# Performance work log

Measured on AMD Instinct MI355X. Metric: run time of the kernel, lower is better.

## Reference

```python
import jax, jax.numpy as jnp
import numpy as np
from jax import lax

B, C, H, W = 32, 3, 256, 256
P, D, E, K = 16, 256, 8, 2
HP, WP = H // P, W // P
N = HP * WP
GATE_IN = C * P * P  # 768
GATE_HID = D // 2    # 128


def _mk(key, shape, scale=0.02):
    return scale * jax.random.normal(key, shape, dtype=jnp.float32)


def setup_inputs() -> dict:
    key = jax.random.key(0)
    ks = jax.random.split(key, 20)
    inp = {
        "x": jax.random.normal(ks[0], (B, C, H, W), dtype=jnp.float32),
        # gate MLP: Linear(768,128) -> ReLU -> Linear(128,8)
        "g_w1": _mk(ks[1], (GATE_HID, GATE_IN)),
        "g_b1": jnp.zeros((GATE_HID,), jnp.float32),
        "g_w2": _mk(ks[2], (E, GATE_HID)),
        "g_b2": jnp.zeros((E,), jnp.float32),
        # per-expert CNN params, stacked with leading expert dim E
        "dw1_w": _mk(ks[3], (E, 3, 1, 3, 3)),   "dw1_b": jnp.zeros((E, 3), jnp.float32),
        "pw1_w": _mk(ks[4], (E, 64, 3, 1, 1)),  "pw1_b": jnp.zeros((E, 64), jnp.float32),
        "dw2_w": _mk(ks[5], (E, 64, 1, 3, 3)),  "dw2_b": jnp.zeros((E, 64), jnp.float32),
        "pw2_w": _mk(ks[6], (E, 128, 64, 1, 1)), "pw2_b": jnp.zeros((E, 128), jnp.float32),
        "dw3_w": _mk(ks[7], (E, 128, 1, 3, 3)), "dw3_b": jnp.zeros((E, 128), jnp.float32),
        "pw3_w": _mk(ks[8], (E, D, 128, 1, 1)), "pw3_b": jnp.zeros((E, D), jnp.float32),
    }
    return inp


def _dwconv(x, w, b, stride):
    # depthwise 3x3, padding 1; x: [n, c, h, w]; w: [c, 1, 3, 3]
    c = x.shape[1]
    y = lax.conv_general_dilated(
        x, w, (stride, stride), ((1, 1), (1, 1)),
        dimension_numbers=("NCHW", "OIHW", "NCHW"), feature_group_count=c)
    return jax.nn.relu(y + b[None, :, None, None])


def _pwconv(x, w, b):
    # pointwise 1x1 conv as GEMM; w: [o, c, 1, 1]
    y = jnp.einsum("nchw,oc->nohw", x, w[:, :, 0, 0]) + b[None, :, None, None]
    return jax.nn.relu(y)


def _expert(x, dw1w, dw1b, pw1w, pw1b, dw2w, dw2b, pw2w, pw2b, dw3w, dw3b, pw3w, pw3b):
    # x: [BN, 3, 16, 16] -> [BN, D]
    x = _pwconv(_dwconv(x, dw1w, dw1b, 2), pw1w, pw1b)   # [BN, 64, 8, 8]
    x = _pwconv(_dwconv(x, dw2w, dw2b, 2), pw2w, pw2b)   # [BN, 128, 4, 4]
    x = _pwconv(_dwconv(x, dw3w, dw3b, 2), pw3w, pw3b)   # [BN, 256, 2, 2]
    return x.mean(axis=(2, 3))                            # adaptive avg pool to 1x1


def reference(x, g_w1, g_b1, g_w2, g_b2,
              dw1_w, dw1_b, pw1_w, pw1_b, dw2_w, dw2_b, pw2_w, pw2_b,
              dw3_w, dw3_b, pw3_w, pw3_b):
    b = x.shape[0]
    # nn.Unfold(kernel=P, stride=P): columns ordered (c, di, dj)
    patches = x.reshape(b, C, HP, P, WP, P).transpose(0, 2, 4, 1, 3, 5)  # [B,hp,wp,C,P,P]
    patches_sp = patches.reshape(b * N, C, P, P)
    patches_flat = patches_sp.reshape(b * N, GATE_IN)

    # gate (eval mode: dropout is identity)
    h = jax.nn.relu(patches_flat @ g_w1.T + g_b1)
    logits = h @ g_w2.T + g_b2                       # [BN, E]
    topk_vals, topk_idx = lax.top_k(logits, K)       # [BN, K]
    weights = jax.nn.softmax(topk_vals, axis=-1)
    one_hot = jax.nn.one_hot(topk_idx, E, dtype=x.dtype)   # [BN, K, E]
    routing = (one_hot * weights[..., None]).sum(axis=1)   # [BN, E]

    # run all experts densely (as the original does), then combine
    expert_outs = jax.vmap(_expert, in_axes=(None,) + (0,) * 12)(
        patches_sp, dw1_w, dw1_b, pw1_w, pw1_b, dw2_w, dw2_b,
        pw2_w, pw2_b, dw3_w, dw3_b, pw3_w, pw3_b)   # [E, BN, D]
    out = jnp.einsum("ne,end->nd", routing, expert_outs)  # [BN, D]

    features = out.reshape(b, HP, WP, D).transpose(0, 3, 1, 2)  # [B, D, hp, wp]
    load_balance_loss = jnp.float32(0.0)  # eval mode
    return features, load_balance_loss
```

## Files before the change

### kernel.cpp

```cpp
#include <hip/hip_runtime.h>

#define BN 8192
#define GIN 768

#define O_ROUTE_I 0UL
#define O_ROUTE_W (O_ROUTE_I + (size_t)BN*2*4)
#define O_COUNTS  (O_ROUTE_W + (size_t)BN*2*4)
#define O_LISTS   (O_COUNTS + 256)
#define O_PW2T    (O_LISTS + (size_t)8*BN*4)
#define O_PW3T    (O_PW2T + (size_t)8*64*128*4)
#define O_SLOT    (O_PW3T + (size_t)8*128*256*4)

__global__ __launch_bounds__(256) void k0_prep(const float* __restrict__ pw2w,
                                               const float* __restrict__ pw3w,
                                               float* __restrict__ pw2t,
                                               float* __restrict__ pw3t,
                                               int* __restrict__ counts)
{
    int tid = blockIdx.x * 256 + threadIdx.x;
    if (tid < 8) counts[tid] = 0;
    for (int idx = tid; idx < 8 * 128 * 64; idx += 256 * 256) {
        int e = idx >> 13; int r = idx & 8191; int oc = r >> 6; int c = r & 63;
        pw2t[(size_t)e * 8192 + c * 128 + oc] = pw2w[idx];
    }
    for (int idx = tid; idx < 8 * 256 * 128; idx += 256 * 256) {
        int e = idx >> 15; int r = idx & 32767; int oc = r >> 7; int c = r & 127;
        pw3t[(size_t)e * 32768 + c * 256 + oc] = pw3w[idx];
    }
}

__global__ __launch_bounds__(256) void k1_gate(
    const float* __restrict__ x, const float* __restrict__ w1,
    const float* __restrict__ b1, const float* __restrict__ w2,
    const float* __restrict__ b2,
    int* __restrict__ route_i, float* __restrict__ route_w,
    int* __restrict__ counts, int* __restrict__ lists)
{
    __shared__ __align__(16) float A[32][44];
    __shared__ __align__(16) float Wl[32][132];
    __shared__ float hl[32][132];
    __shared__ float ll[32][8];

    int tid = threadIdx.x;
    int pblk = blockIdx.x * 32;

    int pgrp = tid & 7;
    int hgrp = tid >> 3;
    float acc[4][4] = {};

    int sp  = tid >> 3;
    int sk4 = (tid & 7) * 4;
    int swh = tid >> 1;
    int swk = (tid & 1) * 16;

    int patchA = pblk + sp;
    int bA = patchA >> 8; int nA = patchA & 255; int hpA = nA >> 4; int wpA = nA & 15;

    for (int kc = 0; kc < GIN; kc += 32) {
        {
            int k = kc + sk4;
            int c = k >> 8; int rem = k & 255; int ri = rem >> 4; int j = rem & 15;
            const float* src = x + (((size_t)(bA * 3 + c) * 256 + hpA * 16 + ri) * 256 + wpA * 16 + j);
            float4 a4 = *reinterpret_cast<const float4*>(src);
            A[sk4 + 0][sp] = a4.x; A[sk4 + 1][sp] = a4.y;
            A[sk4 + 2][sp] = a4.z; A[sk4 + 3][sp] = a4.w;
        }
        {
            const float* wsrc = w1 + (size_t)swh * GIN + kc + swk;
            #pragma unroll
            for (int q = 0; q < 4; q++) {
                float4 w4 = *reinterpret_cast<const float4*>(wsrc + q * 4);
                Wl[swk + q * 4 + 0][swh] = w4.x; Wl[swk + q * 4 + 1][swh] = w4.y;
                Wl[swk + q * 4 + 2][swh] = w4.z; Wl[swk + q * 4 + 3][swh] = w4.w;
            }
        }
        __syncthreads();
        float cacc[4][4] = {};
        #pragma unroll
        for (int k2 = 0; k2 < 32; k2++) {
            float4 av = *reinterpret_cast<const float4*>(&A[k2][pgrp * 4]);
            float4 wv = *reinterpret_cast<const float4*>(&Wl[k2][hgrp * 4]);
            float aa[4] = {av.x, av.y, av.z, av.w};
            float ww[4] = {wv.x, wv.y, wv.z, wv.w};
            #pragma unroll
            for (int i = 0; i < 4; i++) {
                #pragma unroll
                for (int jj = 0; jj < 4; jj++) cacc[i][jj] += aa[i] * ww[jj];
            }
        }
        #pragma unroll
        for (int i = 0; i < 4; i++) {
            #pragma unroll
            for (int jj = 0; jj < 4; jj++) acc[i][jj] += cacc[i][jj];
        }
        __syncthreads();
    }

    #pragma unroll
    for (int jj = 0; jj < 4; jj++) {
        float bb = b1[hgrp * 4 + jj];
        #pragma unroll
        for (int i = 0; i < 4; i++) {
            float v = acc[i][jj] + bb;
            hl[pgrp * 4 + i][hgrp * 4 + jj] = v > 0.f ? v : 0.f;
        }
    }
    __syncthreads();

    {
        int lp = tid >> 3; int le = tid & 7;
        float lacc = b2[le];
        const float* wrow = w2 + le * 128;
        for (int h = 0; h < 128; h++) lacc += hl[lp][h] * wrow[h];
        ll[lp][le] = lacc;
    }
    __syncthreads();

    if (tid < 32) {
        int patch = pblk + tid;
        float v[8];
        #pragma unroll
        for (int e = 0; e < 8; e++) v[e] = ll[tid][e];
        int e0 = 0; float m0 = v[0];
        #pragma unroll
        for (int e = 1; e < 8; e++) if (v[e] > m0) { m0 = v[e]; e0 = e; }
        int e1 = -1; float m1 = -3.0e38f;
        #pragma unroll
        for (int e = 0; e < 8; e++) if (e != e0 && v[e] > m1) { m1 = v[e]; e1 = e; }
        float t = expf(m1 - m0);
        float w0 = 1.f / (1.f + t);
        float w1v = t * w0;
        route_i[patch * 2] = e0; route_i[patch * 2 + 1] = e1;
        route_w[patch * 2] = w0; route_w[patch * 2 + 1] = w1v;
        int p0 = atomicAdd(&counts[e0], 1);
        lists[e0 * BN + p0] = patch * 2;
        int p1 = atomicAdd(&counts[e1], 1);
        lists[e1 * BN + p1] = patch * 2 + 1;
    }
}

__global__ __launch_bounds__(256, 4) void k23_expert(
    const float* __restrict__ x, const int* __restrict__ counts,
    const int* __restrict__ lists,
    const float* __restrict__ dw1w, const float* __restrict__ dw1b,
    const float* __restrict__ pw1w, const float* __restrict__ pw1b,
    const float* __restrict__ dw2w, const float* __restrict__ dw2b,
    const float* __restrict__ pw2t, const float* __restrict__ pw2b,
    const float* __restrict__ dw3w, const float* __restrict__ dw3b,
    const float* __restrict__ pw3t, const float* __restrict__ pw3b,
    float* __restrict__ slot)
{
    __shared__ __align__(16) float buf[4][2560];

    int e = blockIdx.x & 7;
    int chunk = blockIdx.x >> 3;
    int cnt = counts[e];
    int base = chunk * 4;
    if (base >= cnt) return;
    int tid = threadIdx.x;
    int en = tid >> 6; int l = tid & 63;
    if (base + en >= cnt) return;
    int pslot = lists[e * BN + base + en];
    int patch = pslot >> 1;
    int b = patch >> 8, nn = patch & 255, hp = nn >> 4, wp = nn & 15;

    float* pl  = buf[en];
    float* d1  = buf[en] + 2048;
    float* d2t = buf[en];
    float* p2  = buf[en];
    float* d3  = buf[en] + 2048;

    {
        int r = l >> 2; int j4 = (l & 3) * 4;
        #pragma unroll
        for (int c = 0; c < 3; c++) {
            const float* src = x + (((size_t)(b * 3 + c) * 256 + hp * 16 + r) * 256 + wp * 16 + j4);
            float4 v = *reinterpret_cast<const float4*>(src);
            *reinterpret_cast<float4*>(&pl[c * 320 + r * 20 + j4]) = v;
        }
    }

    {
        int oh = l >> 3, ow = l & 7;
        #pragma unroll
        for (int c = 0; c < 3; c++) {
            const float* w9 = dw1w + (e * 3 + c) * 9;
            float acc = dw1b[e * 3 + c];
            #pragma unroll
            for (int ki = 0; ki < 3; ki++) {
                int ih = oh * 2 - 1 + ki;
                if ((unsigned)ih < 16u) {
                    #pragma unroll
                    for (int kj = 0; kj < 3; kj++) {
                        int iw = ow * 2 - 1 + kj;
                        if ((unsigned)iw < 16u) acc += pl[c * 320 + ih * 20 + iw] * w9[ki * 3 + kj];
                    }
                }
            }
            d1[c * 64 + l] = acc > 0.f ? acc : 0.f;
        }
    }

    {
        const float* w3 = pw1w + (e * 64 + l) * 3;
        float pw0 = w3[0], pw1v = w3[1], pw2v = w3[2];
        float pb = pw1b[e * 64 + l];
        const float* w9 = dw2w + (e * 64 + l) * 9;
        float wd[9];
        #pragma unroll
        for (int i = 0; i < 9; i++) wd[i] = w9[i];
        float bd = dw2b[e * 64 + l];

        float rc[8] = {};
        float re[8], ro[8];

        #pragma unroll
        for (int oh = 0; oh < 4; oh++) {
            #pragma unroll
            for (int half = 0; half < 2; half++) {
                float* dst = half ? ro : re;
                const float* d1b = d1 + (oh * 2 + half) * 8;
                float4 x0 = *reinterpret_cast<const float4*>(&d1b[0]);
                float4 x1 = *reinterpret_cast<const float4*>(&d1b[4]);
                float4 y0 = *reinterpret_cast<const float4*>(&d1b[64]);
                float4 y1 = *reinterpret_cast<const float4*>(&d1b[68]);
                float4 z0 = *reinterpret_cast<const float4*>(&d1b[128]);
                float4 z1 = *reinterpret_cast<const float4*>(&d1b[132]);
                float v;
                v = pb + x0.x * pw0 + y0.x * pw1v + z0.x * pw2v; dst[0] = v > 0.f ? v : 0.f;
                v = pb + x0.y * pw0 + y0.y * pw1v + z0.y * pw2v; dst[1] = v > 0.f ? v : 0.f;
                v = pb + x0.z * pw0 + y0.z * pw1v + z0.z * pw2v; dst[2] = v > 0.f ? v : 0.f;
                v = pb + x0.w * pw0 + y0.w * pw1v + z0.w * pw2v; dst[3] = v > 0.f ? v : 0.f;
                v = pb + x1.x * pw0 + y1.x * pw1v + z1.x * pw2v; dst[4] = v > 0.f ? v : 0.f;
                v = pb + x1.y * pw0 + y1.y * pw1v + z1.y * pw2v; dst[5] = v > 0.f ? v : 0.f;
                v = pb + x1.z * pw0 + y1.z * pw1v + z1.z * pw2v; dst[6] = v > 0.f ? v : 0.f;
                v = pb + x1.w * pw0 + y1.w * pw1v + z1.w * pw2v; dst[7] = v > 0.f ? v : 0.f;
            }
            #pragma unroll
            for (int ow = 0; ow < 4; ow++) {
                float acc = bd;
                if (oh > 0) {
                    #pragma unroll
                    for (int kj = 0; kj < 3; kj++) {
                        int iw = ow * 2 - 1 + kj;
                        if ((unsigned)iw < 8u) acc += rc[iw] * wd[kj];
                    }
                }
                #pragma unroll
                for (int kj = 0; kj < 3; kj++) {
                    int iw = ow * 2 - 1 + kj;
                    if ((unsigned)iw < 8u) acc += re[iw] * wd[3 + kj];
                }
                #pragma unroll
                for (int kj = 0; kj < 3; kj++) {
                    int iw = ow * 2 - 1 + kj;
                    if ((unsigned)iw < 8u) acc += ro[iw] * wd[6 + kj];
                }
                d2t[(oh * 4 + ow) * 68 + l] = acc > 0.f ? acc : 0.f;
            }
            #pragma unroll
            for (int i = 0; i < 8; i++) rc[i] = ro[i];
        }
    }

    {
        int ocg = l & 15; int pq = l >> 4;
        int oc0 = ocg * 8; int p0 = pq * 4;
        float acc[8][4] = {};
        const float* wbase = pw2t + (size_t)e * 8192;
        for (int c4 = 0; c4 < 16; c4++) {
            float4 a0 = *reinterpret_cast<const float4*>(&d2t[(p0 + 0) * 68 + c4 * 4]);
            float4 a1 = *reinterpret_cast<const float4*>(&d2t[(p0 + 1) * 68 + c4 * 4]);
            float4 a2 = *reinterpret_cast<const float4*>(&d2t[(p0 + 2) * 68 + c4 * 4]);
            float4 a3 = *reinterpret_cast<const float4*>(&d2t[(p0 + 3) * 68 + c4 * 4]);
            float av[4][4] = {{a0.x, a1.x, a2.x, a3.x}, {a0.y, a1.y, a2.y, a3.y},
                              {a0.z, a1.z, a2.z, a3.z}, {a0.w, a1.w, a2.w, a3.w}};
            #pragma unroll
            for (int cc = 0; cc < 4; cc++) {
                int c = c4 * 4 + cc;
                float4 wa = *reinterpret_cast<const float4*>(wbase + c * 128 + oc0);
                float4 wb = *reinterpret_cast<const float4*>(wbase + c * 128 + oc0 + 4);
                float wv[8] = {wa.x, wa.y, wa.z, wa.w, wb.x, wb.y, wb.z, wb.w};
                #pragma unroll
                for (int j = 0; j < 8; j++) {
                    #pragma unroll
                    for (int i = 0; i < 4; i++) acc[j][i] += wv[j] * av[cc][i];
                }
            }
        }
        #pragma unroll
        for (int j = 0; j < 8; j++) {
            float bb = pw2b[e * 128 + oc0 + j];
            #pragma unroll
            for (int i = 0; i < 4; i++) {
                float v = acc[j][i] + bb;
                p2[(oc0 + j) * 16 + ((p0 + i + ocg) & 15)] = v > 0.f ? v : 0.f;
            }
        }
    }

    {
        #pragma unroll
        for (int chb = 0; chb < 128; chb += 64) {
            int ch = chb + l;
            int grp = ch >> 3;
            const float* w9 = dw3w + (e * 128 + ch) * 9;
            float bb = dw3b[e * 128 + ch];
            #pragma unroll
            for (int pos = 0; pos < 4; pos++) {
                int oh = pos >> 1, ow = pos & 1;
                float acc = bb;
                #pragma unroll
                for (int ki = 0; ki < 3; ki++) {
                    int ih = oh * 2 - 1 + ki;
                    if ((unsigned)ih < 4u) {
                        #pragma unroll
                        for (int kj = 0; kj < 3; kj++) {
                            int iw = ow * 2 - 1 + kj;
                            if ((unsigned)iw < 4u)
                                acc += p2[ch * 16 + ((ih * 4 + iw + grp) & 15)] * w9[ki * 3 + kj];
                        }
                    }
                }
                d3[ch * 4 + pos] = acc > 0.f ? acc : 0.f;
            }
        }
    }

    {
        int oc0 = l * 4;
        const float* wbase = pw3t + (size_t)e * 32768;
        float acc[4][4] = {};
        for (int c = 0; c < 128; c++) {
            float4 a = *reinterpret_cast<const float4*>(&d3[c * 4]);
            float4 w = *reinterpret_cast<const float4*>(wbase + c * 256 + oc0);
            float av[4] = {a.x, a.y, a.z, a.w};
            float wv[4] = {w.x, w.y, w.z, w.w};
            #pragma unroll
            for (int j = 0; j < 4; j++) {
                #pragma unroll
                for (int i = 0; i < 4; i++) acc[j][i] += wv[j] * av[i];
            }
        }
        float o4[4];
        #pragma unroll
        for (int j = 0; j < 4; j++) {
            float bb = pw3b[e * 256 + oc0 + j];
            float s = 0.f;
            #pragma unroll
            for (int i = 0; i < 4; i++) {
                float v = acc[j][i] + bb;
                s += (v > 0.f ? v : 0.f);
            }
            o4[j] = 0.25f * s;
        }
        *reinterpret_cast<float4*>(slot + (size_t)pslot * 256 + oc0) =
            make_float4(o4[0], o4[1], o4[2], o4[3]);
    }
}

__global__ __launch_bounds__(256) void k4_comb(
    const float* __restrict__ slot, const float* __restrict__ route_w,
    float* __restrict__ out)
{
    __shared__ float cl[16][257];
    int bx = blockIdx.x;
    int b = bx >> 4; int hp = bx & 15;
    int tid = threadIdx.x;
    int d = tid;
    for (int wp = 0; wp < 16; wp++) {
        int n = (b * 16 + hp) * 16 + wp;
        float w0 = route_w[n * 2], w1 = route_w[n * 2 + 1];
        float v = w0 * slot[(size_t)(n * 2) * 256 + d] + w1 * slot[(size_t)(n * 2 + 1) * 256 + d];
        cl[wp][d] = v;
    }
    __syncthreads();
    int wp = tid & 15; int dg = tid >> 4;
    for (int r = 0; r < 16; r++) {
        int dd = r * 16 + dg;
        out[(((size_t)b * 256 + dd) * 16 + hp) * 16 + wp] = cl[wp][dd];
    }
    if (bx == 0 && tid == 0) out[(size_t)BN * 256] = 0.0f;
}

extern "C" void kernel_launch(void* const* d_in, const int* in_sizes, int n_in,
                              void* d_out, int out_size, void* d_ws, size_t ws_size,
                              hipStream_t stream)
{
    const float* x    = (const float*)d_in[0];
    const float* gw1  = (const float*)d_in[1];
    const float* gb1  = (const float*)d_in[2];
    const float* gw2  = (const float*)d_in[3];
    const float* gb2  = (const float*)d_in[4];
    const float* dw1w = (const float*)d_in[5];
    const float* dw1b = (const float*)d_in[6];
    const float* pw1w = (const float*)d_in[7];
    const float* pw1b = (const float*)d_in[8];
    const float* dw2w = (const float*)d_in[9];
    const float* dw2b = (const float*)d_in[10];
    const float* pw2w = (const float*)d_in[11];
    const float* pw2b = (const float*)d_in[12];
    const float* dw3w = (const float*)d_in[13];
    const float* dw3b = (const float*)d_in[14];
    const float* pw3w = (const float*)d_in[15];
    const float* pw3b = (const float*)d_in[16];

    char* ws = (char*)d_ws;
    int*   route_i = (int*)(ws + O_ROUTE_I);
    float* route_w = (float*)(ws + O_ROUTE_W);
    int*   counts  = (int*)(ws + O_COUNTS);
    int*   lists   = (int*)(ws + O_LISTS);
    float* pw2t    = (float*)(ws + O_PW2T);
    float* pw3t    = (float*)(ws + O_PW3T);
    float* slot    = (float*)(ws + O_SLOT);
    float* out     = (float*)d_out;

    hipLaunchKernelGGL(k0_prep, dim3(256), dim3(256), 0, stream,
                       pw2w, pw3w, pw2t, pw3t, counts);
    hipLaunchKernelGGL(k1_gate, dim3(BN / 32), dim3(256), 0, stream,
                       x, gw1, gb1, gw2, gb2, route_i, route_w, counts, lists);
    hipLaunchKernelGGL(k23_expert, dim3(8 * 2048), dim3(256), 0, stream,
                       x, counts, lists, dw1w, dw1b, pw1w, pw1b, dw2w, dw2b,
                       pw2t, pw2b, dw3w, dw3b, pw3t, pw3b, slot);
    hipLaunchKernelGGL(k4_comb, dim3(512), dim3(256), 0, stream,
                       slot, route_w, out);
}
```

Before: 532.0 us.

## Share expert pointwise GEMM weights across patches in block and shrink gate tile

In the expert kernel, the pw2 and pw3 pointwise GEMMs are repartitioned. Each wavefront now computes a slice of output channels for all four patches in the block, reading the other wavefronts' activations through shared memory. Before, each wavefront owned one patch and read the full weight matrix. This cuts per-block global weight traffic about fourfold, at the cost of added __syncthreads and rotated/skewed shared-memory indexing to avoid bank conflicts. The gate kernel tile is also halved to 16 patches per block, doubling the grid for more parallelism.

```diff
diff --git a/kernel.cpp b/kernel.cpp
--- a/kernel.cpp
+++ b/kernel.cpp
@@ -2,6 +2,7 @@
 
 #define BN 8192
 #define GIN 768
+#define SL 2560
 
 #define O_ROUTE_I 0UL
 #define O_ROUTE_W (O_ROUTE_I + (size_t)BN*2*4)
@@ -36,20 +37,20 @@
     int* __restrict__ route_i, float* __restrict__ route_w,
     int* __restrict__ counts, int* __restrict__ lists)
 {
-    __shared__ __align__(16) float A[32][44];
+    __shared__ __align__(16) float A[32][20];
     __shared__ __align__(16) float Wl[32][132];
-    __shared__ float hl[32][132];
-    __shared__ float ll[32][8];
+    __shared__ float hl[16][132];
+    __shared__ float ll[16][8];
 
     int tid = threadIdx.x;
-    int pblk = blockIdx.x * 32;
+    int pblk = blockIdx.x * 16;
 
     int pgrp = tid & 7;
     int hgrp = tid >> 3;
-    float acc[4][4] = {};
-
-    int sp  = tid >> 3;
-    int sk4 = (tid & 7) * 4;
+    float acc[2][4] = {};
+
+    int sp  = tid >> 4;
+    int sk2 = (tid & 15) * 2;
     int swh = tid >> 1;
     int swk = (tid & 1) * 16;
 
@@ -58,38 +59,37 @@
 
     for (int kc = 0; kc < GIN; kc += 32) {
         {
-            int k = kc + sk4;
+            int k = kc + sk2;
             int c = k >> 8; int rem = k & 255; int ri = rem >> 4; int j = rem & 15;
             const float* src = x + (((size_t)(bA * 3 + c) * 256 + hpA * 16 + ri) * 256 + wpA * 16 + j);
-            float4 a4 = *reinterpret_cast<const float4*>(src);
-            A[sk4 + 0][sp] = a4.x; A[sk4 + 1][sp] = a4.y;
-            A[sk4 + 2][sp] = a4.z; A[sk4 + 3][sp] = a4.w;
+            float2 a2 = *reinterpret_cast<const float2*>(src);
+            A[sk2][sp] = a2.x; A[sk2 + 1][sp] = a2.y;
         }
         {
             const float* wsrc = w1 + (size_t)swh * GIN + kc + swk;
             #pragma unroll
-            for (int q = 0; q < 4; q++) {
-                float4 w4 = *reinterpret_cast<const float4*>(wsrc + q * 4);
-                Wl[swk + q * 4 + 0][swh] = w4.x; Wl[swk + q * 4 + 1][swh] = w4.y;
-                Wl[swk + q * 4 + 2][swh] = w4.z; Wl[swk + q * 4 + 3][swh] = w4.w;
+            for (int qq = 0; qq < 4; qq++) {
+                float4 w4 = *reinterpret_cast<const float4*>(wsrc + qq * 4);
+                Wl[swk + qq * 4 + 0][swh] = w4.x; Wl[swk + qq * 4 + 1][swh] = w4.y;
+                Wl[swk + qq * 4 + 2][swh] = w4.z; Wl[swk + qq * 4 + 3][swh] = w4.w;
             }
         }
         __syncthreads();
-        float cacc[4][4] = {};
+        float cacc[2][4] = {};
         #pragma unroll
         for (int k2 = 0; k2 < 32; k2++) {
-            float4 av = *reinterpret_cast<const float4*>(&A[k2][pgrp * 4]);
+            float2 av = *reinterpret_cast<const float2*>(&A[k2][pgrp * 2]);
             float4 wv = *reinterpret_cast<const float4*>(&Wl[k2][hgrp * 4]);
-            float aa[4] = {av.x, av.y, av.z, av.w};
+            float aa[2] = {av.x, av.y};
             float ww[4] = {wv.x, wv.y, wv.z, wv.w};
             #pragma unroll
-            for (int i = 0; i < 4; i++) {
+            for (int i = 0; i < 2; i++) {
                 #pragma unroll
                 for (int jj = 0; jj < 4; jj++) cacc[i][jj] += aa[i] * ww[jj];
             }
         }
         #pragma unroll
-        for (int i = 0; i < 4; i++) {
+        for (int i = 0; i < 2; i++) {
             #pragma unroll
             for (int jj = 0; jj < 4; jj++) acc[i][jj] += cacc[i][jj];
         }
@@ -100,14 +100,14 @@
     for (int jj = 0; jj < 4; jj++) {
         float bb = b1[hgrp * 4 + jj];
         #pragma unroll
-        for (int i = 0; i < 4; i++) {
+        for (int i = 0; i < 2; i++) {
             float v = acc[i][jj] + bb;
-            hl[pgrp * 4 + i][hgrp * 4 + jj] = v > 0.f ? v : 0.f;
-        }
-    }
-    __syncthreads();
-
-    {
+            hl[pgrp * 2 + i][hgrp * 4 + jj] = v > 0.f ? v : 0.f;
+        }
+    }
+    __syncthreads();
+
+    if (tid < 128) {
         int lp = tid >> 3; int le = tid & 7;
         float lacc = b2[le];
         const float* wrow = w2 + le * 128;
@@ -116,7 +116,7 @@
     }
     __syncthreads();
 
-    if (tid < 32) {
+    if (tid < 16) {
         int patch = pblk + tid;
         float v[8];
         #pragma unroll
@@ -150,25 +150,28 @@
     const float* __restrict__ pw3t, const float* __restrict__ pw3b,
     float* __restrict__ slot)
 {
-    __shared__ __align__(16) float buf[4][2560];
+    __shared__ __align__(16) float buf[4][SL];
 
     int e = blockIdx.x & 7;
     int chunk = blockIdx.x >> 3;
     int cnt = counts[e];
     int base = chunk * 4;
     if (base >= cnt) return;
+    int n_en = cnt - base; if (n_en > 4) n_en = 4;
     int tid = threadIdx.x;
-    int en = tid >> 6; int l = tid & 63;
-    if (base + en >= cnt) return;
-    int pslot = lists[e * BN + base + en];
+    int wid = tid >> 6;
+    int l = tid & 63;
+    int en_l = l >> 4;
+    int q = l & 15;
+
+    int myidx = base + wid; if (myidx >= cnt) myidx = cnt - 1;
+    int pslot = lists[e * BN + myidx];
     int patch = pslot >> 1;
     int b = patch >> 8, nn = patch & 255, hp = nn >> 4, wp = nn & 15;
 
-    float* pl  = buf[en];
-    float* d1  = buf[en] + 2048;
-    float* d2t = buf[en];
-    float* p2  = buf[en];
-    float* d3  = buf[en] + 2048;
+    float* pl  = buf[wid];
+    float* d1  = buf[wid] + 2048;
+    float* d2t = buf[wid];
 
     {
         int r = l >> 2; int j4 = (l & 3) * 4;
@@ -211,6 +214,7 @@
         for (int i = 0; i < 9; i++) wd[i] = w9[i];
         float bd = dw2b[e * 64 + l];
 
+        int dcol = (l + wid * 4) & 63;
         float rc[8] = {};
         float re[8], ro[8];
 
@@ -256,23 +260,28 @@
                     int iw = ow * 2 - 1 + kj;
                     if ((unsigned)iw < 8u) acc += ro[iw] * wd[6 + kj];
                 }
-                d2t[(oh * 4 + ow) * 68 + l] = acc > 0.f ? acc : 0.f;
+                d2t[(oh * 4 + ow) * 68 + dcol] = acc > 0.f ? acc : 0.f;
             }
             #pragma unroll
             for (int i = 0; i < 8; i++) rc[i] = ro[i];
         }
     }
-
-    {
-        int ocg = l & 15; int pq = l >> 4;
-        int oc0 = ocg * 8; int p0 = pq * 4;
+    __syncthreads();
+
+    {
+        const float* dsl = buf[en_l];
+        int ocg = q & 3, pq = q >> 2;
+        int oc0 = wid * 32 + ocg * 8;
+        int p0 = pq * 4;
         float acc[8][4] = {};
         const float* wbase = pw2t + (size_t)e * 8192;
+        #pragma unroll 2
         for (int c4 = 0; c4 < 16; c4++) {
-            float4 a0 = *reinterpret_cast<const float4*>(&d2t[(p0 + 0) * 68 + c4 * 4]);
-            float4 a1 = *reinterpret_cast<const float4*>(&d2t[(p0 + 1) * 68 + c4 * 4]);
-            float4 a2 = *reinterpret_cast<const float4*>(&d2t[(p0 + 2) * 68 + c4 * 4]);
-            float4 a3 = *reinterpret_cast<const float4*>(&d2t[(p0 + 3) * 68 + c4 * 4]);
+            int col = (c4 * 4 + en_l * 4) & 63;
+            float4 a0 = *reinterpret_cast<const float4*>(&dsl[(p0 + 0) * 68 + col]);
+            float4 a1 = *reinterpret_cast<const float4*>(&dsl[(p0 + 1) * 68 + col]);
+            float4 a2 = *reinterpret_cast<const float4*>(&dsl[(p0 + 2) * 68 + col]);
+            float4 a3 = *reinterpret_cast<const float4*>(&dsl[(p0 + 3) * 68 + col]);
             float av[4][4] = {{a0.x, a1.x, a2.x, a3.x}, {a0.y, a1.y, a2.y, a3.y},
                               {a0.z, a1.z, a2.z, a3.z}, {a0.w, a1.w, a2.w, a3.w}};
             #pragma unroll
@@ -288,18 +297,24 @@
                 }
             }
         }
+        __syncthreads();
+        int g = oc0 >> 3;
+        float* p2w = buf[en_l];
         #pragma unroll
         for (int j = 0; j < 8; j++) {
             float bb = pw2b[e * 128 + oc0 + j];
             #pragma unroll
             for (int i = 0; i < 4; i++) {
                 float v = acc[j][i] + bb;
-                p2[(oc0 + j) * 16 + ((p0 + i + ocg) & 15)] = v > 0.f ? v : 0.f;
-            }
-        }
-    }
-
-    {
+                p2w[(oc0 + j) * 16 + ((p0 + i + g + en_l) & 15)] = v > 0.f ? v : 0.f;
+            }
+        }
+    }
+    __syncthreads();
+
+    {
+        float* p2 = buf[wid];
+        float* d3 = buf[wid] + 2048;
         #pragma unroll
         for (int chb = 0; chb < 128; chb += 64) {
             int ch = chb + l;
@@ -318,21 +333,24 @@
                         for (int kj = 0; kj < 3; kj++) {
                             int iw = ow * 2 - 1 + kj;
                             if ((unsigned)iw < 4u)
-                                acc += p2[ch * 16 + ((ih * 4 + iw + grp) & 15)] * w9[ki * 3 + kj];
+                                acc += p2[ch * 16 + ((ih * 4 + iw + grp + wid) & 15)] * w9[ki * 3 + kj];
                         }
                     }
                 }
-                d3[ch * 4 + pos] = acc > 0.f ? acc : 0.f;
-            }
-        }
-    }
-
-    {
-        int oc0 = l * 4;
+                d3[((ch + wid * 4) & 127) * 4 + pos] = acc > 0.f ? acc : 0.f;
+            }
+        }
+    }
+    __syncthreads();
+
+    {
+        int oc0 = wid * 64 + q * 4;
+        const float* d3b = buf[en_l] + 2048;
         const float* wbase = pw3t + (size_t)e * 32768;
         float acc[4][4] = {};
+        #pragma unroll 4
         for (int c = 0; c < 128; c++) {
-            float4 a = *reinterpret_cast<const float4*>(&d3[c * 4]);
+            float4 a = *reinterpret_cast<const float4*>(&d3b[((c + en_l * 4) & 127) * 4]);
             float4 w = *reinterpret_cast<const float4*>(wbase + c * 256 + oc0);
             float av[4] = {a.x, a.y, a.z, a.w};
             float wv[4] = {w.x, w.y, w.z, w.w};
@@ -342,20 +360,23 @@
                 for (int i = 0; i < 4; i++) acc[j][i] += wv[j] * av[i];
             }
         }
-        float o4[4];
-        #pragma unroll
-        for (int j = 0; j < 4; j++) {
-            float bb = pw3b[e * 256 + oc0 + j];
-            float s = 0.f;
-            #pragma unroll
-            for (int i = 0; i < 4; i++) {
-                float v = acc[j][i] + bb;
-                s += (v > 0.f ? v : 0.f);
-            }
-            o4[j] = 0.25f * s;
-        }
-        *reinterpret_cast<float4*>(slot + (size_t)pslot * 256 + oc0) =
-            make_float4(o4[0], o4[1], o4[2], o4[3]);
+        if (en_l < n_en) {
+            int ps_f = lists[e * BN + base + en_l];
+            float o4[4];
+            #pragma unroll
+            for (int j = 0; j < 4; j++) {
+                float bb = pw3b[e * 256 + oc0 + j];
+                float s = 0.f;
+                #pragma unroll
+                for (int i = 0; i < 4; i++) {
+                    float v = acc[j][i] + bb;
+                    s += (v > 0.f ? v : 0.f);
+                }
+                o4[j] = 0.25f * s;
+            }
+            *reinterpret_cast<float4*>(slot + (size_t)ps_f * 256 + oc0) =
+                make_float4(o4[0], o4[1], o4[2], o4[3]);
+        }
     }
 }
 
@@ -417,7 +438,7 @@
 
     hipLaunchKernelGGL(k0_prep, dim3(256), dim3(256), 0, stream,
                        pw2w, pw3w, pw2t, pw3t, counts);
-    hipLaunchKernelGGL(k1_gate, dim3(BN / 32), dim3(256), 0, stream,
+    hipLaunchKernelGGL(k1_gate, dim3(BN / 16), dim3(256), 0, stream,
                        x, gw1, gb1, gw2, gb2, route_i, route_w, counts, lists);
     hipLaunchKernelGGL(k23_expert, dim3(8 * 2048), dim3(256), 0, stream,
                        x, counts, lists, dw1w, dw1b, pw1w, pw1b, dw2w, dw2b,
```

New measurement: 520.2 us. 1.02x faster.
